# Kernel tuning notes

Hardware: AMD Instinct MI355X
Metric: run time of the kernel (lower is better)

## Reference

```python
import jax, jax.numpy as jnp
from jax import lax
import numpy as np

B, T, R, U = 32, 32, 256, 4  # batch, exposures, recon size, upscale (2**(lambda_scale_factor-1))
YS = R // U                  # yt_img_size = 64


def setup_inputs() -> dict:
    key = jax.random.key(0)
    k = jax.random.split(key, 6)
    yt = jax.random.normal(k[0], (B, T, YS, YS), dtype=jnp.float32)
    Ht = jax.random.normal(k[1], (T, R, R), dtype=jnp.float32) * 0.1
    W1 = jax.random.normal(k[2], (32, 1, 3, 3), dtype=jnp.float32) * 0.1
    b1 = jnp.zeros((32,), dtype=jnp.float32)
    W2 = jax.random.normal(k[3], (1, 32, 3, 3), dtype=jnp.float32) * 0.1
    b2 = jnp.zeros((1,), dtype=jnp.float32)
    return {"yt": yt, "Ht": Ht, "W1": W1, "b1": b1, "W2": W2, "b2": b2}


def _conv(x, w, b):
    # NCHW / OIHW, stride 1, SAME padding
    y = lax.conv_general_dilated(x, w, window_strides=(1, 1), padding="SAME",
                                 dimension_numbers=("NCHW", "OIHW", "NCHW"))
    return y + b[None, :, None, None]


def reference(yt, Ht, W1, b1, W2, b2):
    # Structured A^T @ yt without materializing the (R^2, T*YS^2) sparse matrix:
    # out[b,p,q] = sum_t Ht[t,p,q] * yt[b,t,p//U,q//U]
    yt_up = jnp.repeat(jnp.repeat(yt, U, axis=2), U, axis=3)      # (B,T,R,R) nearest upsample
    x = jnp.einsum("btpq,tpq->bpq", yt_up, Ht)[:, None]            # (B,1,R,R)
    # upsample_postproc_block: Conv(1->32,3x3) -> ReLU -> Conv(32->1,3x3)
    x = jax.nn.relu(_conv(x, W1, b1))
    x = _conv(x, W2, b2)
    return x
```

## Files before the change

kernel.cpp:

```cpp
#include <hip/hip_runtime.h>

#define R 256
#define T 32

#define TROWS 16
#define HC 34
#define HRR 18
#define HSTR 36
#define CP 648
#define WSLICE (4 * CP)
#define NPX (HRR * HC)
#define NPAIR (NPX / 2)

typedef float v2f __attribute__((ext_vector_type(2)));
#define FMA2(a, b, c) __builtin_elementwise_fma((a), (b), (c))

__global__ __launch_bounds__(512) void einsum_kernel(
    const float* __restrict__ yt, const float* __restrict__ Ht,
    float* __restrict__ x) {
  const int bq  = blockIdx.x >> 6;
  const int yy  = blockIdx.x & 63;
  const int b0  = bq * 8;
  const int tid = threadIdx.x;
  const int q   = tid & 255;
  const int rhh = tid >> 8;
  const int q4  = q >> 2;

  __shared__ float yts[8 * 32 * 64];

#pragma unroll
  for (int i = 0; i < 8; ++i) {
    int f4  = tid + i * 512;
    int b_l = f4 >> 9;
    int t   = (f4 >> 4) & 31;
    int xx4 = f4 & 15;
    float4 v = *(const float4*)(yt + (((size_t)(b0 + b_l) * T + t) * 64 + yy) * 64 + xx4 * 4);
    *(float4*)(yts + f4 * 4) = v;
  }
  __syncthreads();

#pragma unroll
  for (int rr = 0; rr < 2; ++rr) {
    const int p = yy * 4 + rhh * 2 + rr;
    float ht[T];
#pragma unroll
    for (int t = 0; t < T; ++t) ht[t] = Ht[((size_t)t * R + p) * R + q];

#pragma unroll
    for (int b_l = 0; b_l < 8; ++b_l) {
      const float* ys = yts + b_l * 2048 + q4;
      float acc = 0.f;
#pragma unroll
      for (int t = 0; t < T; ++t) acc += ht[t] * ys[t * 64];
      x[((size_t)(b0 + b_l) * R + p) * R + q] = acc;
    }
  }
}

template <bool EDGE>
__device__ __forceinline__ void conv_body(
    const v2f (&patch2)[5][9], bool slot4, const bool (&oob)[10],
    const int (&sw)[5], float* hs,
    const float* __restrict__ W1, const float* __restrict__ b1,
    const float* __restrict__ W2, int cl, int hboff, v2f (&acc2)[8][2]) {
  for (int cg = 0; cg < 8; ++cg) {
    float w2[9];
#pragma unroll
    for (int k = 0; k < 9; ++k) w2[k] = W2[(cg * 4 + cl) * 9 + k];

#pragma unroll
    for (int c = 0; c < 4; ++c) {
      const int ch = cg * 4 + c;
      const float bias = b1[ch];
      v2f h[5];
#pragma unroll
      for (int s = 0; s < 5; ++s) h[s] = (v2f){bias, bias};
#pragma unroll
      for (int k = 0; k < 9; ++k) {
        const float w = W1[ch * 9 + k];
        const v2f wv = {w, w};
#pragma unroll
        for (int s = 0; s < 5; ++s) h[s] = FMA2(wv, patch2[s][k], h[s]);
      }
      const v2f z = {0.f, 0.f};
#pragma unroll
      for (int s = 0; s < 5; ++s) h[s] = __builtin_elementwise_max(h[s], z);
      if (EDGE) {
#pragma unroll
        for (int s = 0; s < 5; ++s) {
          if (oob[2 * s])     h[s].x = 0.f;
          if (oob[2 * s + 1]) h[s].y = 0.f;
        }
      }
      float* hp = hs + c * CP;
#pragma unroll
      for (int s = 0; s < 4; ++s) *(v2f*)(hp + sw[s]) = h[s];
      if (slot4) *(v2f*)(hp + sw[4]) = h[4];
    }

#pragma unroll
    for (int j = 0; j < 10; ++j) {
      float4 v4 = *(const float4*)(hs + hboff + j * HSTR);
      float2 vt = *(const float2*)(hs + hboff + j * HSTR + 4);
      v2f P[5];
      P[0] = (v2f){v4.x, v4.y};
      P[1] = (v2f){v4.y, v4.z};
      P[2] = (v2f){v4.z, v4.w};
      P[3] = (v2f){v4.w, vt.x};
      P[4] = (v2f){vt.x, vt.y};
#pragma unroll
      for (int dy = 0; dy < 3; ++dy) {
        int ai = j - dy;
        if (ai >= 0 && ai < 8) {
#pragma unroll
          for (int dx = 0; dx < 3; ++dx) {
            const float w = w2[dy * 3 + dx];
            const v2f wv = {w, w};
            acc2[ai][0] = FMA2(wv, P[dx], acc2[ai][0]);
            acc2[ai][1] = FMA2(wv, P[dx + 2], acc2[ai][1]);
          }
        }
      }
    }
  }
}

template <bool EDGE>
__device__ __forceinline__ void conv_tile(
    const float* __restrict__ xb, int ty0, int ox0, int lane, float* hsw,
    const float* __restrict__ W1, const float* __restrict__ b1,
    const float* __restrict__ W2, const float* __restrict__ b2,
    float* __restrict__ outp) {
  v2f  patch2[5][9];
  int  sw[5];
  bool oob[10];
  const bool slot4 = (lane < NPAIR - 4 * 64);
#pragma unroll
  for (int it = 0; it < 5; ++it) {
    int pi = lane + it * 64;
    bool act = (it < 4) || slot4;
    int px0 = 2 * pi;
    int hy  = act ? (px0 / HC) : 0;
    int hx0 = act ? (px0 % HC) : 0;
    sw[it] = hy * HSTR + hx0;
    int ghy = ty0 - 1 + hy;
    int ghx0 = ox0 - 1 + hx0;
    bool rowok = (ghy >= 0) & (ghy < R);
    oob[2 * it]     = !(rowok & (ghx0 >= 0) & (ghx0 < R));
    oob[2 * it + 1] = !(rowok & (ghx0 + 1 >= 0) & (ghx0 + 1 < R));
#pragma unroll
    for (int ky = 0; ky < 3; ++ky) {
      const int gy  = ty0 - 2 + hy + ky;
      const int gx0 = ox0 - 2 + hx0;
      v2f fa, fb;
      if (EDGE) {
        float xv[4];
#pragma unroll
        for (int c = 0; c < 4; ++c) {
          int gx = gx0 + c;
          bool ok = act & (gy >= 0) & (gy < R) & (gx >= 0) & (gx < R);
          xv[c] = ok ? xb[gy * R + gx] : 0.f;
        }
        fa = (v2f){xv[0], xv[1]};
        fb = (v2f){xv[2], xv[3]};
      } else {
        const float* xp = xb + gy * R + gx0;
        fa = act ? *(const v2f*)(xp)     : (v2f){0.f, 0.f};
        fb = act ? *(const v2f*)(xp + 2) : (v2f){0.f, 0.f};
      }
      patch2[it][3 * ky + 0] = fa;
      patch2[it][3 * ky + 1] = (v2f){fa.y, fb.x};
      patch2[it][3 * ky + 2] = fb;
    }
  }

  const int g  = lane & 7;
  const int cl = (lane >> 3) & 3;
  const int rh = lane >> 5;
  const int r0 = 8 * rh;

  v2f acc2[8][2];
#pragma unroll
  for (int ai = 0; ai < 8; ++ai) {
    acc2[ai][0] = (v2f){0.f, 0.f};
    acc2[ai][1] = (v2f){0.f, 0.f};
  }

  const int hboff = cl * CP + r0 * HSTR + 4 * g;

  conv_body<EDGE>(patch2, slot4, oob, sw, hsw, W1, b1, W2, cl, hboff, acc2);

  const float bias2 = b2[0];
#pragma unroll
  for (int ai = 0; ai < 8; ++ai)
#pragma unroll
    for (int h = 0; h < 2; ++h) {
      float vx = acc2[ai][h].x, vy = acc2[ai][h].y;
      vx += __shfl_xor(vx, 8);  vy += __shfl_xor(vy, 8);
      vx += __shfl_xor(vx, 16); vy += __shfl_xor(vy, 16);
      acc2[ai][h].x = vx; acc2[ai][h].y = vy;
    }
  if (cl == 0) {
#pragma unroll
    for (int ai = 0; ai < 8; ++ai) {
      float4 o = {acc2[ai][0].x + bias2, acc2[ai][0].y + bias2,
                  acc2[ai][1].x + bias2, acc2[ai][1].y + bias2};
      *(float4*)(outp + (ty0 + r0 + ai) * R + ox0 + 4 * g) = o;
    }
  }
}

__global__ __launch_bounds__(128) void conv_fused_kernel(
    const float* __restrict__ x, const float* __restrict__ W1,
    const float* __restrict__ b1, const float* __restrict__ W2,
    const float* __restrict__ b2, float* __restrict__ out) {
  __shared__ float hs[2 * WSLICE];

  const int tid  = threadIdx.x;
  const int lane = tid & 63;
  const int wv   = tid >> 6;
  const int b    = blockIdx.x >> 6;
  const int tile = blockIdx.x & 63;
  const int ty0  = (tile >> 3) * 32 + wv * TROWS;
  const int ox0  = (tile & 7) * 32;
  const float* xb   = x + (size_t)b * R * R;
  float*       outp = out + (size_t)b * R * R;
  float*       hsw  = hs + wv * WSLICE;

  const bool edge = (ty0 == 0) | (ty0 == R - TROWS) | (ox0 == 0) | (ox0 == R - 32);
  if (edge)
    conv_tile<true>(xb, ty0, ox0, lane, hsw, W1, b1, W2, b2, outp);
  else
    conv_tile<false>(xb, ty0, ox0, lane, hsw, W1, b1, W2, b2, outp);
}

extern "C" void kernel_launch(void* const* d_in, const int* in_sizes, int n_in,
                              void* d_out, int out_size, void* d_ws, size_t ws_size,
                              hipStream_t stream) {
  const float* yt = (const float*)d_in[0];
  const float* Ht = (const float*)d_in[1];
  const float* W1 = (const float*)d_in[2];
  const float* b1 = (const float*)d_in[3];
  const float* W2 = (const float*)d_in[4];
  const float* b2 = (const float*)d_in[5];
  float* outp = (float*)d_out;
  float* x    = (float*)d_ws;

  einsum_kernel<<<256, 512, 0, stream>>>(yt, Ht, x);
  conv_fused_kernel<<<2048, 128, 0, stream>>>(x, W1, b1, W2, b2, outp);
}
```

Baseline: 123.4 us.

## Split conv hidden channels across two waves and reduce partials through LDS

```diff
diff --git a/kernel.cpp b/kernel.cpp
--- a/kernel.cpp
+++ b/kernel.cpp
@@ -59,11 +59,11 @@
 
 template <bool EDGE>
 __device__ __forceinline__ void conv_body(
-    const v2f (&patch2)[5][9], bool slot4, const bool (&oob)[10],
+    int cg0, const v2f (&patch2)[5][9], bool slot4, const bool (&oob)[10],
     const int (&sw)[5], float* hs,
     const float* __restrict__ W1, const float* __restrict__ b1,
     const float* __restrict__ W2, int cl, int hboff, v2f (&acc2)[8][2]) {
-  for (int cg = 0; cg < 8; ++cg) {
+  for (int cg = cg0; cg < cg0 + 4; ++cg) {
     float w2[9];
 #pragma unroll
     for (int k = 0; k < 9; ++k) w2[k] = W2[(cg * 4 + cl) * 9 + k];
@@ -127,7 +127,8 @@
 
 template <bool EDGE>
 __device__ __forceinline__ void conv_tile(
-    const float* __restrict__ xb, int ty0, int ox0, int lane, float* hsw,
+    const float* __restrict__ xb, int ty0, int ox0, int lane, int wv,
+    float* hs,
     const float* __restrict__ W1, const float* __restrict__ b1,
     const float* __restrict__ W2, const float* __restrict__ b2,
     float* __restrict__ outp) {
@@ -186,9 +187,33 @@
     acc2[ai][1] = (v2f){0.f, 0.f};
   }
 
+  float* hsw = hs + wv * WSLICE;
   const int hboff = cl * CP + r0 * HSTR + 4 * g;
 
-  conv_body<EDGE>(patch2, slot4, oob, sw, hsw, W1, b1, W2, cl, hboff, acc2);
+  conv_body<EDGE>(4 * wv, patch2, slot4, oob, sw, hsw, W1, b1, W2, cl,
+                  hboff, acc2);
+
+  if (wv == 1) {
+    float* pp = hsw + lane * 34;
+#pragma unroll
+    for (int ai = 0; ai < 8; ++ai) {
+      *(v2f*)(pp + ai * 4)     = acc2[ai][0];
+      *(v2f*)(pp + ai * 4 + 2) = acc2[ai][1];
+    }
+  }
+  __syncthreads();
+  if (wv == 1) return;
+
+  {
+    const float* pp = hs + WSLICE + lane * 34;
+#pragma unroll
+    for (int ai = 0; ai < 8; ++ai) {
+      v2f p0 = *(const v2f*)(pp + ai * 4);
+      v2f p1 = *(const v2f*)(pp + ai * 4 + 2);
+      acc2[ai][0] += p0;
+      acc2[ai][1] += p1;
+    }
+  }
 
   const float bias2 = b2[0];
 #pragma unroll
@@ -219,19 +244,18 @@
   const int tid  = threadIdx.x;
   const int lane = tid & 63;
   const int wv   = tid >> 6;
-  const int b    = blockIdx.x >> 6;
-  const int tile = blockIdx.x & 63;
-  const int ty0  = (tile >> 3) * 32 + wv * TROWS;
+  const int b    = blockIdx.x >> 7;
+  const int tile = blockIdx.x & 127;
+  const int ty0  = (tile >> 3) * TROWS;
   const int ox0  = (tile & 7) * 32;
   const float* xb   = x + (size_t)b * R * R;
   float*       outp = out + (size_t)b * R * R;
-  float*       hsw  = hs + wv * WSLICE;
 
   const bool edge = (ty0 == 0) | (ty0 == R - TROWS) | (ox0 == 0) | (ox0 == R - 32);
   if (edge)
-    conv_tile<true>(xb, ty0, ox0, lane, hsw, W1, b1, W2, b2, outp);
+    conv_tile<true>(xb, ty0, ox0, lane, wv, hs, W1, b1, W2, b2, outp);
   else
-    conv_tile<false>(xb, ty0, ox0, lane, hsw, W1, b1, W2, b2, outp);
+    conv_tile<false>(xb, ty0, ox0, lane, wv, hs, W1, b1, W2, b2, outp);
 }
 
 extern "C" void kernel_launch(void* const* d_in, const int* in_sizes, int n_in,
@@ -247,5 +271,5 @@
   float* x    = (float*)d_ws;
 
   einsum_kernel<<<256, 512, 0, stream>>>(yt, Ht, x);
-  conv_fused_kernel<<<2048, 128, 0, stream>>>(x, W1, b1, W2, b2, outp);
-}
+  conv_fused_kernel<<<4096, 128, 0, stream>>>(x, W1, b1, W2, b2, outp);
+}
```

Result: slower. 138.1 us (+11.9%).
